# Kernel optimization log

Hardware: AMD Instinct MI355X
Metric: run time of the kernel (lower is better)

## Reference

```python
import jax, jax.numpy as jnp
import numpy as np


def setup_inputs() -> dict:
    key = jax.random.key(0)
    k1, k2 = jax.random.split(key)
    N, K, C = 2, 32, 32
    h, w = 64, 64
    H, W = 1024, 1024
    grid = jax.random.normal(k1, (N, K, C, h, w), dtype=jnp.float32)
    guidemap = jax.random.normal(k2, (N, C, H, W), dtype=jnp.float32)
    return {"grid": grid, "guidemap": guidemap}


def reference(grid, guidemap):
    N, C, H, W = guidemap.shape
    h, w = grid.shape[3], grid.shape[4]
    f1, f2 = H // h, W // w
    # F.unfold with kernel==stride (non-overlapping blocks):
    # [N,C,H,W] -> [N,C,f1*f2,h,w] with kernel elements row-major within a block.
    g = guidemap.reshape(N, C, h, f1, w, f2)
    g = g.transpose(0, 1, 3, 5, 2, 4).reshape(N, C, f1 * f2, h, w)
    # Per-location small contraction over channels C.
    out = jnp.einsum('ikjmn,ijlmn->iklmn', grid, g)  # [N,K,f1*f2,h,w]
    # F.fold with kernel==stride (non-overlapping scatter, no overlap-add):
    out = out.reshape(N, -1, f1, f2, h, w)
    out = out.transpose(0, 1, 4, 2, 5, 3).reshape(N, -1, H, W)
    return out
```

## Files before the change

### kernel.cpp

```cpp
#include <hip/hip_runtime.h>


namespace {
constexpr int NIMG = 2;
constexpr int K = 32;
constexpr int C = 32;
constexpr int HB = 64, WB = 64;
constexpr int F1 = 16, F2 = 16;
constexpr int H = 1024, W = 1024;
constexpr int HW = H * W;
}

__global__ __launch_bounds__(512, 4) void gridup_kernel(
    const float* __restrict__ grd,
    const float* __restrict__ gm,
    float* __restrict__ out)
{
    __shared__ float4 sG4[C][64];
    __shared__ float4 sM4[C][K / 4];

    const int b   = blockIdx.x;
    const int n   = b >> 12;
    const int rem = b & 4095;
    const int by  = rem >> 6;
    const int bx  = rem & 63;
    const int t   = threadIdx.x;

    {
        const float* gbase = gm + (size_t)n * C * HW + (by * F1) * W + bx * F2;
        #pragma unroll
        for (int i = 0; i < 4; ++i) {
            const int e   = t + 512 * i;
            const int c   = e >> 6;
            const int l   = e & 63;
            const int r   = l >> 2;
            const int col = (l & 3) << 2;
            sG4[c][l] = *reinterpret_cast<const float4*>(
                gbase + (size_t)c * HW + r * W + col);
        }
    }
    {
        const float* mb = grd + (size_t)n * (K * C * HB * WB) + by * WB + bx;
        float* sMf = reinterpret_cast<float*>(&sM4[0][0]);
        #pragma unroll
        for (int i = 0; i < 2; ++i) {
            const int e = t + 512 * i;
            const int k = e & 31;
            const int c = e >> 5;
            sMf[e] = mb[(size_t)(k * C + c) * (HB * WB)];
        }
    }
    __syncthreads();

    const int kg = t >> 6;
    const int l  = t & 63;

    float acc[4][4] = {};
    #pragma unroll
    for (int c = 0; c < C; ++c) {
        const float4 g = sG4[c][l];
        const float4 m = sM4[c][kg];
        const float gv[4] = {g.x, g.y, g.z, g.w};
        const float mv[4] = {m.x, m.y, m.z, m.w};
        #pragma unroll
        for (int dk = 0; dk < 4; ++dk) {
            #pragma unroll
            for (int p = 0; p < 4; ++p) {
                acc[dk][p] += mv[dk] * gv[p];
            }
        }
    }

    const int r   = l >> 2;
    const int col = (l & 3) << 2;
    float* ob = out + ((size_t)n * K + kg * 4) * HW + (by * F1 + r) * W + bx * F2 + col;
    #pragma unroll
    for (int dk = 0; dk < 4; ++dk) {
        const float4 v = {acc[dk][0], acc[dk][1], acc[dk][2], acc[dk][3]};
        *reinterpret_cast<float4*>(ob + (size_t)dk * HW) = v;
    }
}

extern "C" void kernel_launch(void* const* d_in, const int* in_sizes, int n_in,
                              void* d_out, int out_size, void* d_ws, size_t ws_size,
                              hipStream_t stream) {
    const float* grd = (const float*)d_in[0];
    const float* gm  = (const float*)d_in[1];
    float* out = (float*)d_out;

    const int nblocks = NIMG * HB * WB;
    gridup_kernel<<<nblocks, 512, 0, stream>>>(grd, gm, out);
}
```

Baseline: 190.2 us.

## Make kernel persistent with double-buffered direct global-to-LDS tile staging

Replaces one-block-per-tile launch with 512 persistent workgroups that each process 16 consecutive tiles in the same row. The next tile is prefetched into a second LDS buffer with global_load_lds while the current one is computed, using hand-tuned vmcnt waits. Workgroup-to-range mapping is swizzled across XCDs. This aims to hide load latency and cut per-block launch overhead, but depends on fragile manual waitcnt counts (the output stores also count toward vmcnt) and lowers occupancy.

```diff
diff --git a/kernel.cpp b/kernel.cpp
--- a/kernel.cpp
+++ b/kernel.cpp
@@ -1,83 +1,125 @@
 #include <hip/hip_runtime.h>
+#include <stdint.h>
 
 
 namespace {
-constexpr int NIMG = 2;
-constexpr int K = 32;
-constexpr int C = 32;
-constexpr int HB = 64, WB = 64;
-constexpr int F1 = 16, F2 = 16;
+constexpr int NIMG = 2, K = 32, C = 32;
+constexpr int HB = 64, WB = 64, F1 = 16, F2 = 16;
 constexpr int H = 1024, W = 1024;
 constexpr int HW = H * W;
+constexpr int TILES_TOTAL = NIMG * HB * WB;
+constexpr int NWG = 512;
+constexpr int TPW = TILES_TOTAL / NWG;
+constexpr int GUIDE_F = C * F1 * F2;
+constexpr int MAT_F = K * C;
+constexpr int BUF_F = GUIDE_F + MAT_F;
 }
 
-__global__ __launch_bounds__(512, 4) void gridup_kernel(
+__device__ __forceinline__ void gl_lds16(const float* src, float* dst) {
+    __builtin_amdgcn_global_load_lds(
+        (const __attribute__((address_space(1))) void*)src,
+        (__attribute__((address_space(3))) void*)dst, 16, 0, 0);
+}
+__device__ __forceinline__ void gl_lds4(const float* src, float* dst) {
+    __builtin_amdgcn_global_load_lds(
+        (const __attribute__((address_space(1))) void*)src,
+        (__attribute__((address_space(3))) void*)dst, 4, 0, 0);
+}
+
+__device__ __forceinline__ void stage_tile(const float* __restrict__ gm_n,
+                                           const float* __restrict__ grd_n,
+                                           float* buf, int by, int bx, int t) {
+    const float* gbase = gm_n + (by * F1) * W + bx * F2;
+#pragma unroll
+    for (int i = 0; i < 4; ++i) {
+        const int e = t + 512 * i;
+        const int c = e >> 6;
+        const int l = e & 63;
+        const int r = l >> 2;
+        const int col = (l & 3) << 2;
+        gl_lds16(gbase + (size_t)c * HW + r * W + col, buf + 4 * e);
+    }
+    const float* mb = grd_n + by * WB + bx;
+#pragma unroll
+    for (int i = 0; i < 2; ++i) {
+        const int e = t + 512 * i;
+        const int k = e & 31;
+        const int c = e >> 5;
+        gl_lds4(mb + (size_t)(k * C + c) * (HB * WB), buf + GUIDE_F + e);
+    }
+}
+
+__device__ __forceinline__ void compute_store(const float* buf,
+                                              float* __restrict__ out_n,
+                                              int by, int bx, int kg, int l) {
+    const float4* G = (const float4*)buf;
+    const float4* M = (const float4*)(buf + GUIDE_F);
+    float acc[4][4] = {};
+#pragma unroll
+    for (int c = 0; c < C; ++c) {
+        const float4 g = G[c * 64 + l];
+        const float4 m = M[c * 8 + kg];
+        const float gv[4] = {g.x, g.y, g.z, g.w};
+        const float mv[4] = {m.x, m.y, m.z, m.w};
+#pragma unroll
+        for (int dk = 0; dk < 4; ++dk)
+#pragma unroll
+            for (int p = 0; p < 4; ++p) acc[dk][p] += mv[dk] * gv[p];
+    }
+    const int r = l >> 2;
+    const int col = (l & 3) << 2;
+    float* ob = out_n + (size_t)(kg * 4) * HW + (by * F1 + r) * W + bx * F2 + col;
+#pragma unroll
+    for (int dk = 0; dk < 4; ++dk) {
+        const float4 v = {acc[dk][0], acc[dk][1], acc[dk][2], acc[dk][3]};
+        *reinterpret_cast<float4*>(ob + (size_t)dk * HW) = v;
+    }
+}
+
+__global__ __launch_bounds__(512, 2) void gridup_kernel(
     const float* __restrict__ grd,
     const float* __restrict__ gm,
     float* __restrict__ out)
 {
-    __shared__ float4 sG4[C][64];
-    __shared__ float4 sM4[C][K / 4];
+    __shared__ float lds[2][BUF_F];
 
-    const int b   = blockIdx.x;
-    const int n   = b >> 12;
-    const int rem = b & 4095;
-    const int by  = rem >> 6;
-    const int bx  = rem & 63;
-    const int t   = threadIdx.x;
+    const int wg = blockIdx.x;
+    const int range = (wg & 7) * 64 + (wg >> 3);
+    const int tile0 = range * TPW;
+    const int t = threadIdx.x;
+    const int kg = t >> 6;
+    const int l = t & 63;
 
-    {
-        const float* gbase = gm + (size_t)n * C * HW + (by * F1) * W + bx * F2;
-        #pragma unroll
-        for (int i = 0; i < 4; ++i) {
-            const int e   = t + 512 * i;
-            const int c   = e >> 6;
-            const int l   = e & 63;
-            const int r   = l >> 2;
-            const int col = (l & 3) << 2;
-            sG4[c][l] = *reinterpret_cast<const float4*>(
-                gbase + (size_t)c * HW + r * W + col);
+    const int n = tile0 >> 12;
+    const int rem = tile0 & 4095;
+    const int by = rem >> 6;
+    const int bx0 = rem & 63;
+
+    const float* gm_n = gm + (size_t)n * C * HW;
+    const float* grd_n = grd + (size_t)n * (K * C * HB * WB);
+    float* out_n = out + (size_t)n * K * HW;
+
+    stage_tile(gm_n, grd_n, lds[0], by, bx0, t);
+
+    int cur = 0;
+#pragma unroll 1
+    for (int i = 0; i < TPW; ++i) {
+        if (i + 1 < TPW) {
+            stage_tile(gm_n, grd_n, lds[cur ^ 1], by, bx0 + i + 1, t);
+            if (i == 0) asm volatile("s_waitcnt vmcnt(6)" ::: "memory");
+            else        asm volatile("s_waitcnt vmcnt(10)" ::: "memory");
+        } else {
+            asm volatile("s_waitcnt vmcnt(4)" ::: "memory");
         }
-    }
-    {
-        const float* mb = grd + (size_t)n * (K * C * HB * WB) + by * WB + bx;
-        float* sMf = reinterpret_cast<float*>(&sM4[0][0]);
-        #pragma unroll
-        for (int i = 0; i < 2; ++i) {
-            const int e = t + 512 * i;
-            const int k = e & 31;
-            const int c = e >> 5;
-            sMf[e] = mb[(size_t)(k * C + c) * (HB * WB)];
-        }
-    }
-    __syncthreads();
+        __builtin_amdgcn_s_barrier();
+        asm volatile("" ::: "memory");
 
-    const int kg = t >> 6;
-    const int l  = t & 63;
+        compute_store(lds[cur], out_n, by, bx0 + i, kg, l);
 
-    float acc[4][4] = {};
-    #pragma unroll
-    for (int c = 0; c < C; ++c) {
-        const float4 g = sG4[c][l];
-        const float4 m = sM4[c][kg];
-        const float gv[4] = {g.x, g.y, g.z, g.w};
-        const float mv[4] = {m.x, m.y, m.z, m.w};
-        #pragma unroll
-        for (int dk = 0; dk < 4; ++dk) {
-            #pragma unroll
-            for (int p = 0; p < 4; ++p) {
-                acc[dk][p] += mv[dk] * gv[p];
-            }
-        }
-    }
-
-    const int r   = l >> 2;
-    const int col = (l & 3) << 2;
-    float* ob = out + ((size_t)n * K + kg * 4) * HW + (by * F1 + r) * W + bx * F2 + col;
-    #pragma unroll
-    for (int dk = 0; dk < 4; ++dk) {
-        const float4 v = {acc[dk][0], acc[dk][1], acc[dk][2], acc[dk][3]};
-        *reinterpret_cast<float4*>(ob + (size_t)dk * HW) = v;
+        asm volatile("s_waitcnt lgkmcnt(0)" ::: "memory");
+        __builtin_amdgcn_s_barrier();
+        asm volatile("" ::: "memory");
+        cur ^= 1;
     }
 }
 
@@ -88,6 +130,5 @@
     const float* gm  = (const float*)d_in[1];
     float* out = (float*)d_out;
 
-    const int nblocks = NIMG * HB * WB;
-    gridup_kernel<<<nblocks, 512, 0, stream>>>(grd, gm, out);
+    gridup_kernel<<<NWG, 512, 0, stream>>>(grd, gm, out);
 }
```

After: 194.6 us. +2.3%, slower.
